# Kernel tuning notes

Measured on AMD Instinct MI355X. Metric: run time of the kernel, lower is better.

The kernel has to match this reference:

```python
import jax, jax.numpy as jnp
import numpy as np

N_EXPERTS = 9
MODEL_DIM = 256
NUM_HEADS = 4
N_TOKENS = 4096
LN_EPS = 1e-5


def setup_inputs() -> dict:
    key0 = jax.random.key(0)
    ks = jax.random.split(key0, 8)
    D, E = MODEL_DIM, N_EXPERTS
    x = jax.random.normal(ks[0], (N_TOKENS, D), dtype=jnp.float32)
    label = jax.random.randint(ks[1], (N_TOKENS,), 0, E, dtype=jnp.int64)
    s = 0.02
    Wq = jax.random.normal(ks[2], (E, D, D), dtype=jnp.float32) * s
    Wk = jax.random.normal(ks[3], (E, D, D), dtype=jnp.float32) * s
    Wv = jax.random.normal(ks[4], (E, D, D), dtype=jnp.float32) * s
    bq = jnp.zeros((E, D), dtype=jnp.float32)
    bk = jnp.zeros((E, D), dtype=jnp.float32)
    bv = jnp.zeros((E, D), dtype=jnp.float32)
    Wf = jax.random.normal(ks[5], (D, D), dtype=jnp.float32) * s
    bf = jnp.zeros((D,), dtype=jnp.float32)
    gamma = jnp.ones((D,), dtype=jnp.float32)
    beta = jnp.zeros((D,), dtype=jnp.float32)
    return {"x": x, "label": label, "Wq": Wq, "bq": bq, "Wk": Wk, "bk": bk,
            "Wv": Wv, "bv": bv, "Wf": Wf, "bf": bf, "gamma": gamma, "beta": beta}


def reference(x, label, Wq, bq, Wk, bk, Wv, bv, Wf, bf, gamma, beta):
    # v2 path: per-label expert QKV projection + within-label self-attention.
    N, D = x.shape
    H = NUM_HEADS
    dph = D // H  # dim_per_head = 64
    # NOTE: source uses scale = (dim_per_head // num_heads) ** -0.5
    scale = float((dph // H)) ** -0.5
    idx = jnp.arange(N)
    lbl = label.astype(jnp.int32)

    # Compute all 9 expert projections, then select per-token (dense dispatch).
    q = jnp.einsum('nd,edh->enh', x, Wq)[lbl, idx] + bq[lbl]  # [N, D]
    k = jnp.einsum('nd,edh->enh', x, Wk)[lbl, idx] + bk[lbl]
    v = jnp.einsum('nd,edh->enh', x, Wv)[lbl, idx] + bv[lbl]

    qh = q.reshape(N, H, dph)
    kh = k.reshape(N, H, dph)
    vh = v.reshape(N, H, dph)

    # Attention restricted to tokens with the same label (equivalent to the
    # per-label gather -> bmm -> scatter in the torch loop).
    scores = jnp.einsum('nhd,mhd->hnm', qh, kh) * scale  # [H, N, N]
    same = (lbl[:, None] == lbl[None, :])  # [N, N]
    scores = jnp.where(same[None, :, :], scores, -jnp.inf)
    attn = jax.nn.softmax(scores, axis=-1)
    ctx = jnp.einsum('hnm,mhd->nhd', attn, vh).reshape(N, D)

    out = ctx @ Wf + bf
    h = x + out  # residual is the (gathered) original key
    mean = jnp.mean(h, axis=-1, keepdims=True)
    var = jnp.mean(jnp.square(h - mean), axis=-1, keepdims=True)
    return gamma * (h - mean) / jnp.sqrt(var + LN_EPS) + beta
```

## Files before the change

kernel.cpp:

```cpp
#include <hip/hip_runtime.h>
#include <math.h>

#define N_TOK 4096
#define DIM 256
#define NHEAD 4
#define DPH 64
#define NEXP 9
#define SCALE 0.25f
#define TQ 16
#define MAXST 80
#define GPAD 4736
#define VPITCH 4736

typedef short s8 __attribute__((ext_vector_type(8)));
typedef short s4 __attribute__((ext_vector_type(4)));
typedef float f4 __attribute__((ext_vector_type(4)));

static __device__ __forceinline__ short f2bf(float f) {
  union { float f; unsigned u; } v;
  v.f = f;
  unsigned r = (v.u + 0x7FFFu + ((v.u >> 16) & 1u)) >> 16;
  return (short)r;
}

static __device__ __forceinline__ float wave_sum(float v) {
#pragma unroll
  for (int o = 32; o > 0; o >>= 1) v += __shfl_xor(v, o, 64);
  return v;
}

__global__ void k_build(const int* __restrict__ label, int* __restrict__ perm,
                        int* __restrict__ iperm, int* __restrict__ gs,
                        int* __restrict__ gep, int* __restrict__ st_e,
                        int* __restrict__ st_row, int* __restrict__ nstp) {
  __shared__ int cnt[NEXP];
  __shared__ int base[NEXP];
  int tid = threadIdx.x;
  if (tid < NEXP) cnt[tid] = 0;
  __syncthreads();
  for (int t = tid; t < N_TOK; t += 256) atomicAdd(&cnt[label[t]], 1);
  __syncthreads();
  if (tid == 0) {
    int run = 0, ns = 0;
    for (int e = 0; e < NEXP; e++) {
      gs[e] = run;
      base[e] = run;
      int end = run + cnt[e];
      gep[e] = end;
      for (int r = run; r < end; r += 64) { st_e[ns] = e; st_row[ns] = r; ns++; }
      run = (end + 63) & ~63;
    }
    *nstp = ns;
  }
  __syncthreads();
  for (int t = tid; t < N_TOK; t += 256) {
    int e = label[t];
    int pos = atomicAdd(&base[e], 1);
    perm[pos] = t;
    iperm[t] = pos;
  }
}

__global__ __launch_bounds__(256) void k_castx(const float* __restrict__ x,
                                               const int* __restrict__ perm,
                                               const int* __restrict__ gs,
                                               const int* __restrict__ gep,
                                               short* __restrict__ xb) {
  int grow = blockIdx.x * 64 + (threadIdx.x >> 2);
  int qd = (threadIdx.x & 3) * 64;
  bool valid = false;
#pragma unroll
  for (int e = 0; e < NEXP; e++) valid |= (grow >= gs[e] && grow < gep[e]);
  short* dst = xb + (size_t)grow * DIM + qd;
  if (valid) {
    const float* src = x + (size_t)perm[grow] * DIM + qd;
#pragma unroll
    for (int i = 0; i < 16; i++) {
      float4 v = *(const float4*)(src + i * 4);
      s4 o;
      o[0] = f2bf(v.x); o[1] = f2bf(v.y); o[2] = f2bf(v.z); o[3] = f2bf(v.w);
      *(s4*)(dst + i * 4) = o;
    }
  } else {
#pragma unroll
    for (int i = 0; i < 16; i++) *(s4*)(dst + i * 4) = (s4){0, 0, 0, 0};
  }
}

__global__ __launch_bounds__(256) void k_castw(const float* __restrict__ Wq,
                                               const float* __restrict__ Wk,
                                               const float* __restrict__ Wv,
                                               const float* __restrict__ Wf,
                                               short* __restrict__ WbT) {
  __shared__ short tile[64 * 68];
  int slab = blockIdx.y;
  const float* src;
  if (slab < 9) src = Wq + (size_t)slab * 65536;
  else if (slab < 18) src = Wk + (size_t)(slab - 9) * 65536;
  else if (slab < 27) src = Wv + (size_t)(slab - 18) * 65536;
  else src = Wf;
  int d0 = (blockIdx.x >> 2) * 64, h0 = (blockIdx.x & 3) * 64;
  int tid = threadIdx.x;
  int rl = tid >> 4;
  int hh = (tid & 15) * 4;
#pragma unroll
  for (int p = 0; p < 4; p++) {
    int dl = p * 16 + rl;
    float4 v = *(const float4*)(src + (size_t)(d0 + dl) * 256 + h0 + hh);
    s4 o;
    o[0] = f2bf(v.x); o[1] = f2bf(v.y); o[2] = f2bf(v.z); o[3] = f2bf(v.w);
    *(s4*)&tile[dl * 68 + hh] = o;
  }
  __syncthreads();
  int h = tid >> 2, dq = (tid & 3) * 16;
  s8 pa, pb;
#pragma unroll
  for (int i = 0; i < 8; i++) {
    pa[i] = tile[(dq + i) * 68 + h];
    pb[i] = tile[(dq + 8 + i) * 68 + h];
  }
  short* dst = WbT + (size_t)slab * 65536 + (size_t)(h0 + h) * 256 + d0 + dq;
  *(s8*)dst = pa;
  *(s8*)(dst + 8) = pb;
}

__global__ __launch_bounds__(256) void k_proj(
    const short* __restrict__ xb, const short* __restrict__ WbT,
    const float* __restrict__ bq, const float* __restrict__ bk,
    const float* __restrict__ bv, const int* __restrict__ st_e,
    const int* __restrict__ st_row, const int* __restrict__ nstp,
    short* __restrict__ qg, short* __restrict__ kg, short* __restrict__ vgT) {
  int b = blockIdx.x;
  if (b >= *nstp) return;
  int gy = blockIdx.y;
  int mtx = blockIdx.z;
  int e = st_e[b];
  int row0 = st_row[b];
  int tid = threadIdx.x, wl = tid >> 6, lane = tid & 63;
  int m = lane & 15, quad = lane >> 4;

  const short* Ap = xb + (size_t)(row0 + wl * 16 + m) * DIM + quad * 8;
  const short* Bp = WbT + (size_t)(mtx * 9 + e) * 65536 +
                    (size_t)(gy * 64 + m) * 256 + quad * 8;
  const float* bias = (mtx == 0) ? bq : (mtx == 1) ? bk : bv;

  s8 ac = *(const s8*)Ap;
  s8 bc[4];
#pragma unroll
  for (int t = 0; t < 4; t++) bc[t] = *(const s8*)(Bp + t * 16 * 256);

  f4 acc[4];
#pragma unroll
  for (int t = 0; t < 4; t++) acc[t] = (f4){0.f, 0.f, 0.f, 0.f};

#pragma unroll
  for (int kc = 0; kc < 8; kc++) {
    s8 an = ac;
    s8 bn[4] = {bc[0], bc[1], bc[2], bc[3]};
    if (kc < 7) {
      an = *(const s8*)(Ap + (kc + 1) * 32);
#pragma unroll
      for (int t = 0; t < 4; t++)
        bn[t] = *(const s8*)(Bp + t * 16 * 256 + (kc + 1) * 32);
    }
#pragma unroll
    for (int t = 0; t < 4; t++)
      acc[t] = __builtin_amdgcn_mfma_f32_16x16x32_bf16(ac, bc[t], acc[t], 0, 0, 0);
    ac = an;
#pragma unroll
    for (int t = 0; t < 4; t++) bc[t] = bn[t];
  }

#pragma unroll
  for (int t = 0; t < 4; t++) {
    int col = gy * 64 + t * 16 + m;
    float bs = bias[e * DIM + col];
#pragma unroll
    for (int r = 0; r < 4; r++) {
      int grow = row0 + wl * 16 + quad * 4 + r;
      short o = f2bf(acc[t][r] + bs);
      if (mtx == 2) vgT[(size_t)col * VPITCH + grow] = o;
      else if (mtx == 1) kg[(size_t)grow * DIM + col] = o;
      else qg[(size_t)grow * DIM + col] = o;
    }
  }
}

__global__ __launch_bounds__(256) void k_attn(
    const short* __restrict__ qg, const short* __restrict__ kg,
    const short* __restrict__ vgT, const int* __restrict__ gs,
    const int* __restrict__ gep, const int* __restrict__ st_e,
    const int* __restrict__ st_row, const int* __restrict__ nstp,
    short* __restrict__ cg) {
  int b = blockIdx.x;
  if (b >= *nstp) return;
  int h = blockIdx.y;
  int e = st_e[b];
  int row0 = st_row[b];
  int g0 = gs[e], kend = gep[e];

  int tid = threadIdx.x;
  int wl = tid >> 6;
  int lane = tid & 63;
  int m = lane & 15;
  int quad = lane >> 4;
  int r0 = tid >> 3;
  int c0 = (tid & 7) * 8;

  __shared__ short k_s[64 * 72];
  __shared__ short v_s[64 * 72];
  __shared__ short p_s[4 * 16 * 72];

  int qrow = row0 + wl * 16 + m;
  if (qrow >= kend) qrow = row0;
  s8 qf0 = *(const s8*)&qg[(size_t)qrow * DIM + h * DPH + quad * 8];
  s8 qf1 = *(const s8*)&qg[(size_t)qrow * DIM + h * DPH + 32 + quad * 8];

  f4 o_acc[4];
  float l_r[4];
#pragma unroll
  for (int t = 0; t < 4; t++) o_acc[t] = (f4){0.f, 0.f, 0.f, 0.f};
#pragma unroll
  for (int r = 0; r < 4; r++) l_r[r] = 0.f;

  s8 pk0, pk1, pv0, pv1;
#define PREF(JT)                                                            \
  do {                                                                      \
    pk0 = *(const s8*)&kg[(size_t)((JT) + r0) * DIM + h * DPH + c0];        \
    pk1 = *(const s8*)&kg[(size_t)((JT) + r0 + 32) * DIM + h * DPH + c0];   \
    pv0 = *(const s8*)&vgT[(size_t)(h * DPH + r0) * VPITCH + (JT) + c0];    \
    pv1 = *(const s8*)&vgT[(size_t)(h * DPH + r0 + 32) * VPITCH + (JT) + c0]; \
  } while (0)

  PREF(g0);
  for (int jt = g0; jt < kend; jt += 64) {
    __syncthreads();
    *(s8*)&k_s[r0 * 72 + c0] = pk0;
    *(s8*)&k_s[(r0 + 32) * 72 + c0] = pk1;
    *(s8*)&v_s[r0 * 72 + c0] = pv0;
    *(s8*)&v_s[(r0 + 32) * 72 + c0] = pv1;
    int jn = jt + 64;
    if (jn < kend) PREF(jn);
    __syncthreads();

    f4 s_acc[4];
#pragma unroll
    for (int t = 0; t < 4; t++) s_acc[t] = (f4){0.f, 0.f, 0.f, 0.f};
#pragma unroll
    for (int t = 0; t < 4; t++) {
      s8 kb0 = *(s8*)&k_s[(t * 16 + m) * 72 + quad * 8];
      s8 kb1 = *(s8*)&k_s[(t * 16 + m) * 72 + 32 + quad * 8];
      s_acc[t] = __builtin_amdgcn_mfma_f32_16x16x32_bf16(qf0, kb0, s_acc[t], 0, 0, 0);
      s_acc[t] = __builtin_amdgcn_mfma_f32_16x16x32_bf16(qf1, kb1, s_acc[t], 0, 0, 0);
    }

#pragma unroll
    for (int t = 0; t < 4; t++) {
      bool ok = (jt + t * 16 + m) < kend;
#pragma unroll
      for (int r = 0; r < 4; r++) {
        float p = ok ? __expf(s_acc[t][r] * SCALE) : 0.f;
        l_r[r] += p;
        p_s[(wl * 16 + quad * 4 + r) * 72 + t * 16 + m] = f2bf(p);
      }
    }

#pragma unroll
    for (int kk = 0; kk < 2; kk++) {
      s8 pa = *(s8*)&p_s[(wl * 16 + m) * 72 + kk * 32 + quad * 8];
#pragma unroll
      for (int t = 0; t < 4; t++) {
        s8 vb = *(s8*)&v_s[(t * 16 + m) * 72 + kk * 32 + quad * 8];
        o_acc[t] = __builtin_amdgcn_mfma_f32_16x16x32_bf16(pa, vb, o_acc[t], 0, 0, 0);
      }
    }
  }
#undef PREF

#pragma unroll
  for (int r = 0; r < 4; r++) {
    float lt = l_r[r];
#pragma unroll
    for (int o = 8; o > 0; o >>= 1) lt += __shfl_xor(lt, o, 64);
    float inv = 1.f / lt;
    int grow = row0 + wl * 16 + quad * 4 + r;
#pragma unroll
    for (int t = 0; t < 4; t++)
      cg[(size_t)grow * DIM + h * DPH + t * 16 + m] = f2bf(o_acc[t][r] * inv);
  }
}

__global__ __launch_bounds__(256) void k_out(
    const short* __restrict__ cg, const short* __restrict__ WbT,
    const float* __restrict__ x, const float* __restrict__ bfv,
    const float* __restrict__ gamma, const float* __restrict__ beta,
    const int* __restrict__ iperm, float* __restrict__ out) {
  int t0 = blockIdx.x * TQ;
  int tid = threadIdx.x, wl = tid >> 6, lane = tid & 63;
  int m = lane & 15, quad = lane >> 4;
  __shared__ float h_s[TQ * 260];

  const short* Ap = cg + (size_t)iperm[t0 + m] * DIM + quad * 8;
  const short* Bp = WbT + (size_t)27 * 65536 + (size_t)(wl * 64 + m) * 256 + quad * 8;

  s8 ac = *(const s8*)Ap;
  s8 bc[4];
#pragma unroll
  for (int t = 0; t < 4; t++) bc[t] = *(const s8*)(Bp + t * 16 * 256);

  f4 acc[4];
#pragma unroll
  for (int t = 0; t < 4; t++) acc[t] = (f4){0.f, 0.f, 0.f, 0.f};

#pragma unroll
  for (int kc = 0; kc < 8; kc++) {
    s8 an = ac;
    s8 bn[4] = {bc[0], bc[1], bc[2], bc[3]};
    if (kc < 7) {
      an = *(const s8*)(Ap + (kc + 1) * 32);
#pragma unroll
      for (int t = 0; t < 4; t++)
        bn[t] = *(const s8*)(Bp + t * 16 * 256 + (kc + 1) * 32);
    }
#pragma unroll
    for (int t = 0; t < 4; t++)
      acc[t] = __builtin_amdgcn_mfma_f32_16x16x32_bf16(ac, bc[t], acc[t], 0, 0, 0);
    ac = an;
#pragma unroll
    for (int t = 0; t < 4; t++) bc[t] = bn[t];
  }

#pragma unroll
  for (int t = 0; t < 4; t++) {
    int col = wl * 64 + t * 16 + m;
    float bs = bfv[col];
#pragma unroll
    for (int r = 0; r < 4; r++) h_s[(quad * 4 + r) * 260 + col] = acc[t][r] + bs;
  }
  __syncthreads();

  int w = tid >> 6;
#pragma unroll
  for (int rr = 0; rr < 4; rr++) {
    int row = w * 4 + rr;
    float hv[4];
#pragma unroll
    for (int k2 = 0; k2 < 4; k2++)
      hv[k2] = h_s[row * 260 + lane + 64 * k2] +
               x[(size_t)(t0 + row) * DIM + lane + 64 * k2];
    float sum = hv[0] + hv[1] + hv[2] + hv[3];
    float mean = wave_sum(sum) * (1.f / 256.f);
    float sq = 0.f;
#pragma unroll
    for (int k2 = 0; k2 < 4; k2++) {
      float dd = hv[k2] - mean;
      sq += dd * dd;
    }
    float var = wave_sum(sq) * (1.f / 256.f);
    float rstd = rsqrtf(var + 1e-5f);
#pragma unroll
    for (int k2 = 0; k2 < 4; k2++) {
      int c = lane + 64 * k2;
      out[(size_t)(t0 + row) * DIM + c] =
          gamma[c] * ((hv[k2] - mean) * rstd) + beta[c];
    }
  }
}

extern "C" void kernel_launch(void* const* d_in, const int* in_sizes, int n_in,
                              void* d_out, int out_size, void* d_ws,
                              size_t ws_size, hipStream_t stream) {
  const float* x = (const float*)d_in[0];
  const int* label = (const int*)d_in[1];
  const float* Wq = (const float*)d_in[2];
  const float* bq = (const float*)d_in[3];
  const float* Wk = (const float*)d_in[4];
  const float* bk = (const float*)d_in[5];
  const float* Wv = (const float*)d_in[6];
  const float* bv = (const float*)d_in[7];
  const float* Wf = (const float*)d_in[8];
  const float* bfv = (const float*)d_in[9];
  const float* gamma = (const float*)d_in[10];
  const float* beta = (const float*)d_in[11];
  float* out = (float*)d_out;

  int* perm = (int*)d_ws;
  int* iperm = perm + 8192;
  int* gs = iperm + 4096;
  int* gep = gs + 16;
  int* st_e = gep + 16;
  int* st_row = st_e + 128;
  int* nstp = st_row + 128;
  short* qg = (short*)((char*)d_ws + 65536);
  short* kg = qg + (size_t)GPAD * DIM;
  short* vgT = kg + (size_t)GPAD * DIM;
  short* WbT = vgT + (size_t)DIM * VPITCH;
  short* xb = WbT + (size_t)28 * 65536;
  short* cg = xb;

  hipLaunchKernelGGL(k_build, dim3(1), dim3(256), 0, stream, label, perm,
                     iperm, gs, gep, st_e, st_row, nstp);
  hipLaunchKernelGGL(k_castw, dim3(16, 28), dim3(256), 0, stream, Wq, Wk, Wv,
                     Wf, WbT);
  hipLaunchKernelGGL(k_castx, dim3(GPAD / 64), dim3(256), 0, stream, x, perm,
                     gs, gep, xb);
  hipLaunchKernelGGL(k_proj, dim3(MAXST, 4, 3), dim3(256), 0, stream, xb, WbT,
                     bq, bk, bv, st_e, st_row, nstp, qg, kg, vgT);
  hipLaunchKernelGGL(k_attn, dim3(MAXST, NHEAD), dim3(256), 0, stream, qg, kg,
                     vgT, gs, gep, st_e, st_row, nstp, cg);
  hipLaunchKernelGGL(k_out, dim3(N_TOK / TQ), dim3(256), 0, stream, cg, WbT, x,
                     bfv, gamma, beta, iperm, out);
}
```

Measured before the change: 147.6 us.

## Fuse all stages into one persistent kernel with software grid barriers

Replaces six separate kernel launches with a single persistent kernel of 256 blocks. Work items are handed out grid-stride and the stages are separated by atomic-counter grid barriers. The goal is to remove launch overhead and inter-kernel gaps. The cost is spin-wait barriers, reduced parallelism in the attention stage (nst*4 work items over 256 blocks), and block 0 doing label bucketing serially while the others cast weights. It relies on all 256 blocks being co-resident, and cg now gets its own buffer instead of aliasing xb.

```diff
diff --git a/kernel.cpp b/kernel.cpp
--- a/kernel.cpp
+++ b/kernel.cpp
@@ -7,10 +7,9 @@
 #define DPH 64
 #define NEXP 9
 #define SCALE 0.25f
-#define TQ 16
-#define MAXST 80
 #define GPAD 4736
 #define VPITCH 4736
+#define NB 256
 
 typedef short s8 __attribute__((ext_vector_type(8)));
 typedef short s4 __attribute__((ext_vector_type(4)));
@@ -29,340 +28,333 @@
   return v;
 }
 
-__global__ void k_build(const int* __restrict__ label, int* __restrict__ perm,
-                        int* __restrict__ iperm, int* __restrict__ gs,
-                        int* __restrict__ gep, int* __restrict__ st_e,
-                        int* __restrict__ st_row, int* __restrict__ nstp) {
-  __shared__ int cnt[NEXP];
-  __shared__ int base[NEXP];
+static __device__ __forceinline__ void gridbar(int* c, int target) {
+  __syncthreads();
+  if (threadIdx.x == 0) {
+    __threadfence();
+    __hip_atomic_fetch_add(c, 1, __ATOMIC_RELEASE, __HIP_MEMORY_SCOPE_AGENT);
+    while (__hip_atomic_load(c, __ATOMIC_ACQUIRE, __HIP_MEMORY_SCOPE_AGENT) <
+           target)
+      __builtin_amdgcn_s_sleep(2);
+    __threadfence();
+  }
+  __syncthreads();
+}
+
+__global__ __launch_bounds__(256) void k_fused(
+    const float* __restrict__ x, const int* __restrict__ label,
+    const float* __restrict__ Wq, const float* __restrict__ bq,
+    const float* __restrict__ Wk, const float* __restrict__ bk,
+    const float* __restrict__ Wv, const float* __restrict__ bv,
+    const float* __restrict__ Wf, const float* __restrict__ bfv,
+    const float* __restrict__ gamma, const float* __restrict__ beta,
+    int* __restrict__ cnt, int* __restrict__ perm, int* __restrict__ iperm,
+    int* __restrict__ gs, int* __restrict__ gep, int* __restrict__ st_e,
+    int* __restrict__ st_row, int* __restrict__ nstp, short* __restrict__ qg,
+    short* __restrict__ kg, short* __restrict__ vgT, short* __restrict__ WbT,
+    short* __restrict__ xb, short* __restrict__ cg, float* __restrict__ out) {
+  __shared__ __align__(16) char smem[27648];
+  __shared__ int cntL[NEXP], baseL[NEXP];
+
+  int b = blockIdx.x;
   int tid = threadIdx.x;
-  if (tid < NEXP) cnt[tid] = 0;
-  __syncthreads();
-  for (int t = tid; t < N_TOK; t += 256) atomicAdd(&cnt[label[t]], 1);
-  __syncthreads();
-  if (tid == 0) {
-    int run = 0, ns = 0;
-    for (int e = 0; e < NEXP; e++) {
-      gs[e] = run;
-      base[e] = run;
-      int end = run + cnt[e];
-      gep[e] = end;
-      for (int r = run; r < end; r += 64) { st_e[ns] = e; st_row[ns] = r; ns++; }
-      run = (end + 63) & ~63;
-    }
-    *nstp = ns;
-  }
-  __syncthreads();
-  for (int t = tid; t < N_TOK; t += 256) {
-    int e = label[t];
-    int pos = atomicAdd(&base[e], 1);
-    perm[pos] = t;
-    iperm[t] = pos;
-  }
-}
-
-__global__ __launch_bounds__(256) void k_castx(const float* __restrict__ x,
-                                               const int* __restrict__ perm,
-                                               const int* __restrict__ gs,
-                                               const int* __restrict__ gep,
-                                               short* __restrict__ xb) {
-  int grow = blockIdx.x * 64 + (threadIdx.x >> 2);
-  int qd = (threadIdx.x & 3) * 64;
-  bool valid = false;
-#pragma unroll
-  for (int e = 0; e < NEXP; e++) valid |= (grow >= gs[e] && grow < gep[e]);
-  short* dst = xb + (size_t)grow * DIM + qd;
-  if (valid) {
-    const float* src = x + (size_t)perm[grow] * DIM + qd;
-#pragma unroll
-    for (int i = 0; i < 16; i++) {
-      float4 v = *(const float4*)(src + i * 4);
-      s4 o;
-      o[0] = f2bf(v.x); o[1] = f2bf(v.y); o[2] = f2bf(v.z); o[3] = f2bf(v.w);
-      *(s4*)(dst + i * 4) = o;
+  int wl = tid >> 6, lane = tid & 63;
+  int m = lane & 15, quad = lane >> 4;
+
+  if (b == 0) {
+    if (tid < NEXP) cntL[tid] = 0;
+    __syncthreads();
+    for (int t = tid; t < N_TOK; t += 256) atomicAdd(&cntL[label[t]], 1);
+    __syncthreads();
+    if (tid == 0) {
+      int run = 0, ns = 0;
+      for (int e = 0; e < NEXP; e++) {
+        gs[e] = run;
+        baseL[e] = run;
+        int end = run + cntL[e];
+        gep[e] = end;
+        for (int r = run; r < end; r += 64) {
+          st_e[ns] = e;
+          st_row[ns] = r;
+          ns++;
+        }
+        run = (end + 63) & ~63;
+      }
+      *nstp = ns;
+    }
+    __syncthreads();
+    for (int t = tid; t < N_TOK; t += 256) {
+      int e = label[t];
+      int pos = atomicAdd(&baseL[e], 1);
+      perm[pos] = t;
+      iperm[t] = pos;
     }
   } else {
-#pragma unroll
-    for (int i = 0; i < 16; i++) *(s4*)(dst + i * 4) = (s4){0, 0, 0, 0};
-  }
-}
-
-__global__ __launch_bounds__(256) void k_castw(const float* __restrict__ Wq,
-                                               const float* __restrict__ Wk,
-                                               const float* __restrict__ Wv,
-                                               const float* __restrict__ Wf,
-                                               short* __restrict__ WbT) {
-  __shared__ short tile[64 * 68];
-  int slab = blockIdx.y;
-  const float* src;
-  if (slab < 9) src = Wq + (size_t)slab * 65536;
-  else if (slab < 18) src = Wk + (size_t)(slab - 9) * 65536;
-  else if (slab < 27) src = Wv + (size_t)(slab - 18) * 65536;
-  else src = Wf;
-  int d0 = (blockIdx.x >> 2) * 64, h0 = (blockIdx.x & 3) * 64;
-  int tid = threadIdx.x;
-  int rl = tid >> 4;
-  int hh = (tid & 15) * 4;
-#pragma unroll
-  for (int p = 0; p < 4; p++) {
-    int dl = p * 16 + rl;
-    float4 v = *(const float4*)(src + (size_t)(d0 + dl) * 256 + h0 + hh);
-    s4 o;
-    o[0] = f2bf(v.x); o[1] = f2bf(v.y); o[2] = f2bf(v.z); o[3] = f2bf(v.w);
-    *(s4*)&tile[dl * 68 + hh] = o;
-  }
-  __syncthreads();
-  int h = tid >> 2, dq = (tid & 3) * 16;
-  s8 pa, pb;
-#pragma unroll
-  for (int i = 0; i < 8; i++) {
-    pa[i] = tile[(dq + i) * 68 + h];
-    pb[i] = tile[(dq + 8 + i) * 68 + h];
-  }
-  short* dst = WbT + (size_t)slab * 65536 + (size_t)(h0 + h) * 256 + d0 + dq;
-  *(s8*)dst = pa;
-  *(s8*)(dst + 8) = pb;
-}
-
-__global__ __launch_bounds__(256) void k_proj(
-    const short* __restrict__ xb, const short* __restrict__ WbT,
-    const float* __restrict__ bq, const float* __restrict__ bk,
-    const float* __restrict__ bv, const int* __restrict__ st_e,
-    const int* __restrict__ st_row, const int* __restrict__ nstp,
-    short* __restrict__ qg, short* __restrict__ kg, short* __restrict__ vgT) {
-  int b = blockIdx.x;
-  if (b >= *nstp) return;
-  int gy = blockIdx.y;
-  int mtx = blockIdx.z;
-  int e = st_e[b];
-  int row0 = st_row[b];
-  int tid = threadIdx.x, wl = tid >> 6, lane = tid & 63;
-  int m = lane & 15, quad = lane >> 4;
-
-  const short* Ap = xb + (size_t)(row0 + wl * 16 + m) * DIM + quad * 8;
-  const short* Bp = WbT + (size_t)(mtx * 9 + e) * 65536 +
-                    (size_t)(gy * 64 + m) * 256 + quad * 8;
-  const float* bias = (mtx == 0) ? bq : (mtx == 1) ? bk : bv;
-
-  s8 ac = *(const s8*)Ap;
-  s8 bc[4];
-#pragma unroll
-  for (int t = 0; t < 4; t++) bc[t] = *(const s8*)(Bp + t * 16 * 256);
-
-  f4 acc[4];
-#pragma unroll
-  for (int t = 0; t < 4; t++) acc[t] = (f4){0.f, 0.f, 0.f, 0.f};
-
-#pragma unroll
-  for (int kc = 0; kc < 8; kc++) {
-    s8 an = ac;
-    s8 bn[4] = {bc[0], bc[1], bc[2], bc[3]};
-    if (kc < 7) {
-      an = *(const s8*)(Ap + (kc + 1) * 32);
+    short* tile = (short*)smem;
+    for (int vt = b - 1; vt < 448; vt += NB - 1) {
+      int slab = vt >> 4;
+      const float* src = (slab < 9)    ? Wq + (size_t)slab * 65536
+                         : (slab < 18) ? Wk + (size_t)(slab - 9) * 65536
+                         : (slab < 27) ? Wv + (size_t)(slab - 18) * 65536
+                                       : Wf;
+      int xy = vt & 15;
+      int d0 = (xy >> 2) * 64, h0 = (xy & 3) * 64;
+      int rl = tid >> 4;
+      int hh = (tid & 15) * 4;
+#pragma unroll
+      for (int p = 0; p < 4; p++) {
+        int dl = p * 16 + rl;
+        float4 v = *(const float4*)(src + (size_t)(d0 + dl) * 256 + h0 + hh);
+        s4 o;
+        o[0] = f2bf(v.x); o[1] = f2bf(v.y); o[2] = f2bf(v.z); o[3] = f2bf(v.w);
+        *(s4*)&tile[dl * 68 + hh] = o;
+      }
+      __syncthreads();
+      int h = tid >> 2, dq = (tid & 3) * 16;
+      s8 pa, pb;
+#pragma unroll
+      for (int i = 0; i < 8; i++) {
+        pa[i] = tile[(dq + i) * 68 + h];
+        pb[i] = tile[(dq + 8 + i) * 68 + h];
+      }
+      short* dst = WbT + (size_t)slab * 65536 + (size_t)(h0 + h) * 256 + d0 + dq;
+      *(s8*)dst = pa;
+      *(s8*)(dst + 8) = pb;
+      __syncthreads();
+    }
+  }
+  gridbar(cnt, NB);
+
+  for (int vb = b; vb < GPAD / 64; vb += NB) {
+    int grow = vb * 64 + (tid >> 2);
+    int qd = (tid & 3) * 64;
+    bool valid = false;
+#pragma unroll
+    for (int e = 0; e < NEXP; e++) valid |= (grow >= gs[e] && grow < gep[e]);
+    short* dst = xb + (size_t)grow * DIM + qd;
+    if (valid) {
+      const float* src = x + (size_t)perm[grow] * DIM + qd;
+#pragma unroll
+      for (int i = 0; i < 16; i++) {
+        float4 v = *(const float4*)(src + i * 4);
+        s4 o;
+        o[0] = f2bf(v.x); o[1] = f2bf(v.y); o[2] = f2bf(v.z); o[3] = f2bf(v.w);
+        *(s4*)(dst + i * 4) = o;
+      }
+    } else {
+#pragma unroll
+      for (int i = 0; i < 16; i++) *(s4*)(dst + i * 4) = (s4){0, 0, 0, 0};
+    }
+  }
+  gridbar(cnt, 2 * NB);
+  int nst = *nstp;
+
+  for (int vb = b; vb < nst * 12; vb += NB) {
+    int st = vb / 12, rem = vb - st * 12;
+    int gy = rem & 3, mtx = rem >> 2;
+    int e = st_e[st], row0 = st_row[st];
+    const short* Ap = xb + (size_t)(row0 + wl * 16 + m) * DIM + quad * 8;
+    const short* Bp = WbT + (size_t)(mtx * 9 + e) * 65536 +
+                      (size_t)(gy * 64 + m) * 256 + quad * 8;
+    const float* bias = (mtx == 0) ? bq : (mtx == 1) ? bk : bv;
+
+    s8 ac = *(const s8*)Ap;
+    s8 bc[4];
+#pragma unroll
+    for (int t = 0; t < 4; t++) bc[t] = *(const s8*)(Bp + t * 16 * 256);
+    f4 acc[4];
+#pragma unroll
+    for (int t = 0; t < 4; t++) acc[t] = (f4){0.f, 0.f, 0.f, 0.f};
+#pragma unroll
+    for (int kc = 0; kc < 8; kc++) {
+      s8 an = ac;
+      s8 bn[4] = {bc[0], bc[1], bc[2], bc[3]};
+      if (kc < 7) {
+        an = *(const s8*)(Ap + (kc + 1) * 32);
+#pragma unroll
+        for (int t = 0; t < 4; t++)
+          bn[t] = *(const s8*)(Bp + t * 16 * 256 + (kc + 1) * 32);
+      }
 #pragma unroll
       for (int t = 0; t < 4; t++)
-        bn[t] = *(const s8*)(Bp + t * 16 * 256 + (kc + 1) * 32);
-    }
-#pragma unroll
-    for (int t = 0; t < 4; t++)
-      acc[t] = __builtin_amdgcn_mfma_f32_16x16x32_bf16(ac, bc[t], acc[t], 0, 0, 0);
-    ac = an;
-#pragma unroll
-    for (int t = 0; t < 4; t++) bc[t] = bn[t];
-  }
-
-#pragma unroll
-  for (int t = 0; t < 4; t++) {
-    int col = gy * 64 + t * 16 + m;
-    float bs = bias[e * DIM + col];
-#pragma unroll
-    for (int r = 0; r < 4; r++) {
-      int grow = row0 + wl * 16 + quad * 4 + r;
-      short o = f2bf(acc[t][r] + bs);
-      if (mtx == 2) vgT[(size_t)col * VPITCH + grow] = o;
-      else if (mtx == 1) kg[(size_t)grow * DIM + col] = o;
-      else qg[(size_t)grow * DIM + col] = o;
-    }
-  }
-}
-
-__global__ __launch_bounds__(256) void k_attn(
-    const short* __restrict__ qg, const short* __restrict__ kg,
-    const short* __restrict__ vgT, const int* __restrict__ gs,
-    const int* __restrict__ gep, const int* __restrict__ st_e,
-    const int* __restrict__ st_row, const int* __restrict__ nstp,
-    short* __restrict__ cg) {
-  int b = blockIdx.x;
-  if (b >= *nstp) return;
-  int h = blockIdx.y;
-  int e = st_e[b];
-  int row0 = st_row[b];
-  int g0 = gs[e], kend = gep[e];
-
-  int tid = threadIdx.x;
-  int wl = tid >> 6;
-  int lane = tid & 63;
-  int m = lane & 15;
-  int quad = lane >> 4;
-  int r0 = tid >> 3;
-  int c0 = (tid & 7) * 8;
-
-  __shared__ short k_s[64 * 72];
-  __shared__ short v_s[64 * 72];
-  __shared__ short p_s[4 * 16 * 72];
-
-  int qrow = row0 + wl * 16 + m;
-  if (qrow >= kend) qrow = row0;
-  s8 qf0 = *(const s8*)&qg[(size_t)qrow * DIM + h * DPH + quad * 8];
-  s8 qf1 = *(const s8*)&qg[(size_t)qrow * DIM + h * DPH + 32 + quad * 8];
-
-  f4 o_acc[4];
-  float l_r[4];
-#pragma unroll
-  for (int t = 0; t < 4; t++) o_acc[t] = (f4){0.f, 0.f, 0.f, 0.f};
-#pragma unroll
-  for (int r = 0; r < 4; r++) l_r[r] = 0.f;
-
-  s8 pk0, pk1, pv0, pv1;
-#define PREF(JT)                                                            \
-  do {                                                                      \
-    pk0 = *(const s8*)&kg[(size_t)((JT) + r0) * DIM + h * DPH + c0];        \
-    pk1 = *(const s8*)&kg[(size_t)((JT) + r0 + 32) * DIM + h * DPH + c0];   \
-    pv0 = *(const s8*)&vgT[(size_t)(h * DPH + r0) * VPITCH + (JT) + c0];    \
+        acc[t] = __builtin_amdgcn_mfma_f32_16x16x32_bf16(ac, bc[t], acc[t], 0, 0, 0);
+      ac = an;
+#pragma unroll
+      for (int t = 0; t < 4; t++) bc[t] = bn[t];
+    }
+#pragma unroll
+    for (int t = 0; t < 4; t++) {
+      int col = gy * 64 + t * 16 + m;
+      float bs = bias[e * DIM + col];
+#pragma unroll
+      for (int r = 0; r < 4; r++) {
+        int grow = row0 + wl * 16 + quad * 4 + r;
+        short o = f2bf(acc[t][r] + bs);
+        if (mtx == 2) vgT[(size_t)col * VPITCH + grow] = o;
+        else if (mtx == 1) kg[(size_t)grow * DIM + col] = o;
+        else qg[(size_t)grow * DIM + col] = o;
+      }
+    }
+  }
+  gridbar(cnt, 3 * NB);
+
+  {
+    short* k_s = (short*)smem;
+    short* v_s = (short*)(smem + 9216);
+    short* p_s = (short*)(smem + 18432);
+    int r0 = tid >> 3;
+    int c0 = (tid & 7) * 8;
+    for (int vb = b; vb < nst * 4; vb += NB) {
+      int st = vb >> 2, h = vb & 3;
+      int e = st_e[st], row0 = st_row[st];
+      int g0 = gs[e], kend = gep[e];
+
+      int qrow = row0 + wl * 16 + m;
+      if (qrow >= kend) qrow = row0;
+      s8 qf0 = *(const s8*)&qg[(size_t)qrow * DIM + h * DPH + quad * 8];
+      s8 qf1 = *(const s8*)&qg[(size_t)qrow * DIM + h * DPH + 32 + quad * 8];
+
+      f4 o_acc[4];
+      float l_r[4];
+#pragma unroll
+      for (int t = 0; t < 4; t++) o_acc[t] = (f4){0.f, 0.f, 0.f, 0.f};
+#pragma unroll
+      for (int r = 0; r < 4; r++) l_r[r] = 0.f;
+
+      s8 pk0, pk1, pv0, pv1;
+#define PREF(JT)                                                              \
+  do {                                                                        \
+    pk0 = *(const s8*)&kg[(size_t)((JT) + r0) * DIM + h * DPH + c0];          \
+    pk1 = *(const s8*)&kg[(size_t)((JT) + r0 + 32) * DIM + h * DPH + c0];     \
+    pv0 = *(const s8*)&vgT[(size_t)(h * DPH + r0) * VPITCH + (JT) + c0];      \
     pv1 = *(const s8*)&vgT[(size_t)(h * DPH + r0 + 32) * VPITCH + (JT) + c0]; \
   } while (0)
 
-  PREF(g0);
-  for (int jt = g0; jt < kend; jt += 64) {
+      PREF(g0);
+      for (int jt = g0; jt < kend; jt += 64) {
+        __syncthreads();
+        *(s8*)&k_s[r0 * 72 + c0] = pk0;
+        *(s8*)&k_s[(r0 + 32) * 72 + c0] = pk1;
+        *(s8*)&v_s[r0 * 72 + c0] = pv0;
+        *(s8*)&v_s[(r0 + 32) * 72 + c0] = pv1;
+        int jn = jt + 64;
+        if (jn < kend) PREF(jn);
+        __syncthreads();
+
+        f4 s_acc[4];
+#pragma unroll
+        for (int t = 0; t < 4; t++) s_acc[t] = (f4){0.f, 0.f, 0.f, 0.f};
+#pragma unroll
+        for (int t = 0; t < 4; t++) {
+          s8 kb0 = *(s8*)&k_s[(t * 16 + m) * 72 + quad * 8];
+          s8 kb1 = *(s8*)&k_s[(t * 16 + m) * 72 + 32 + quad * 8];
+          s_acc[t] = __builtin_amdgcn_mfma_f32_16x16x32_bf16(qf0, kb0, s_acc[t], 0, 0, 0);
+          s_acc[t] = __builtin_amdgcn_mfma_f32_16x16x32_bf16(qf1, kb1, s_acc[t], 0, 0, 0);
+        }
+
+#pragma unroll
+        for (int t = 0; t < 4; t++) {
+          bool ok = (jt + t * 16 + m) < kend;
+#pragma unroll
+          for (int r = 0; r < 4; r++) {
+            float p = ok ? __expf(s_acc[t][r] * SCALE) : 0.f;
+            l_r[r] += p;
+            p_s[(wl * 16 + quad * 4 + r) * 72 + t * 16 + m] = f2bf(p);
+          }
+        }
+
+#pragma unroll
+        for (int kk = 0; kk < 2; kk++) {
+          s8 pa = *(s8*)&p_s[(wl * 16 + m) * 72 + kk * 32 + quad * 8];
+#pragma unroll
+          for (int t = 0; t < 4; t++) {
+            s8 vb2 = *(s8*)&v_s[(t * 16 + m) * 72 + kk * 32 + quad * 8];
+            o_acc[t] = __builtin_amdgcn_mfma_f32_16x16x32_bf16(pa, vb2, o_acc[t], 0, 0, 0);
+          }
+        }
+      }
+#undef PREF
+
+#pragma unroll
+      for (int r = 0; r < 4; r++) {
+        float lt = l_r[r];
+#pragma unroll
+        for (int o = 8; o > 0; o >>= 1) lt += __shfl_xor(lt, o, 64);
+        float inv = 1.f / lt;
+        int grow = row0 + wl * 16 + quad * 4 + r;
+#pragma unroll
+        for (int t = 0; t < 4; t++)
+          cg[(size_t)grow * DIM + h * DPH + t * 16 + m] = f2bf(o_acc[t][r] * inv);
+      }
+    }
+  }
+  gridbar(cnt, 4 * NB);
+
+  {
+    float* h_s = (float*)smem;
+    int t0 = b * 16;
+    const short* Ap = cg + (size_t)iperm[t0 + m] * DIM + quad * 8;
+    const short* Bp = WbT + (size_t)27 * 65536 + (size_t)(wl * 64 + m) * 256 + quad * 8;
+
+    s8 ac = *(const s8*)Ap;
+    s8 bc[4];
+#pragma unroll
+    for (int t = 0; t < 4; t++) bc[t] = *(const s8*)(Bp + t * 16 * 256);
+    f4 acc[4];
+#pragma unroll
+    for (int t = 0; t < 4; t++) acc[t] = (f4){0.f, 0.f, 0.f, 0.f};
+#pragma unroll
+    for (int kc = 0; kc < 8; kc++) {
+      s8 an = ac;
+      s8 bn[4] = {bc[0], bc[1], bc[2], bc[3]};
+      if (kc < 7) {
+        an = *(const s8*)(Ap + (kc + 1) * 32);
+#pragma unroll
+        for (int t = 0; t < 4; t++)
+          bn[t] = *(const s8*)(Bp + t * 16 * 256 + (kc + 1) * 32);
+      }
+#pragma unroll
+      for (int t = 0; t < 4; t++)
+        acc[t] = __builtin_amdgcn_mfma_f32_16x16x32_bf16(ac, bc[t], acc[t], 0, 0, 0);
+      ac = an;
+#pragma unroll
+      for (int t = 0; t < 4; t++) bc[t] = bn[t];
+    }
+
+#pragma unroll
+    for (int t = 0; t < 4; t++) {
+      int col = wl * 64 + t * 16 + m;
+      float bs = bfv[col];
+#pragma unroll
+      for (int r = 0; r < 4; r++)
+        h_s[(quad * 4 + r) * 260 + col] = acc[t][r] + bs;
+    }
     __syncthreads();
-    *(s8*)&k_s[r0 * 72 + c0] = pk0;
-    *(s8*)&k_s[(r0 + 32) * 72 + c0] = pk1;
-    *(s8*)&v_s[r0 * 72 + c0] = pv0;
-    *(s8*)&v_s[(r0 + 32) * 72 + c0] = pv1;
-    int jn = jt + 64;
-    if (jn < kend) PREF(jn);
-    __syncthreads();
-
-    f4 s_acc[4];
-#pragma unroll
-    for (int t = 0; t < 4; t++) s_acc[t] = (f4){0.f, 0.f, 0.f, 0.f};
-#pragma unroll
-    for (int t = 0; t < 4; t++) {
-      s8 kb0 = *(s8*)&k_s[(t * 16 + m) * 72 + quad * 8];
-      s8 kb1 = *(s8*)&k_s[(t * 16 + m) * 72 + 32 + quad * 8];
-      s_acc[t] = __builtin_amdgcn_mfma_f32_16x16x32_bf16(qf0, kb0, s_acc[t], 0, 0, 0);
-      s_acc[t] = __builtin_amdgcn_mfma_f32_16x16x32_bf16(qf1, kb1, s_acc[t], 0, 0, 0);
-    }
-
-#pragma unroll
-    for (int t = 0; t < 4; t++) {
-      bool ok = (jt + t * 16 + m) < kend;
-#pragma unroll
-      for (int r = 0; r < 4; r++) {
-        float p = ok ? __expf(s_acc[t][r] * SCALE) : 0.f;
-        l_r[r] += p;
-        p_s[(wl * 16 + quad * 4 + r) * 72 + t * 16 + m] = f2bf(p);
-      }
-    }
-
-#pragma unroll
-    for (int kk = 0; kk < 2; kk++) {
-      s8 pa = *(s8*)&p_s[(wl * 16 + m) * 72 + kk * 32 + quad * 8];
-#pragma unroll
-      for (int t = 0; t < 4; t++) {
-        s8 vb = *(s8*)&v_s[(t * 16 + m) * 72 + kk * 32 + quad * 8];
-        o_acc[t] = __builtin_amdgcn_mfma_f32_16x16x32_bf16(pa, vb, o_acc[t], 0, 0, 0);
-      }
-    }
-  }
-#undef PREF
-
-#pragma unroll
-  for (int r = 0; r < 4; r++) {
-    float lt = l_r[r];
-#pragma unroll
-    for (int o = 8; o > 0; o >>= 1) lt += __shfl_xor(lt, o, 64);
-    float inv = 1.f / lt;
-    int grow = row0 + wl * 16 + quad * 4 + r;
-#pragma unroll
-    for (int t = 0; t < 4; t++)
-      cg[(size_t)grow * DIM + h * DPH + t * 16 + m] = f2bf(o_acc[t][r] * inv);
-  }
-}
-
-__global__ __launch_bounds__(256) void k_out(
-    const short* __restrict__ cg, const short* __restrict__ WbT,
-    const float* __restrict__ x, const float* __restrict__ bfv,
-    const float* __restrict__ gamma, const float* __restrict__ beta,
-    const int* __restrict__ iperm, float* __restrict__ out) {
-  int t0 = blockIdx.x * TQ;
-  int tid = threadIdx.x, wl = tid >> 6, lane = tid & 63;
-  int m = lane & 15, quad = lane >> 4;
-  __shared__ float h_s[TQ * 260];
-
-  const short* Ap = cg + (size_t)iperm[t0 + m] * DIM + quad * 8;
-  const short* Bp = WbT + (size_t)27 * 65536 + (size_t)(wl * 64 + m) * 256 + quad * 8;
-
-  s8 ac = *(const s8*)Ap;
-  s8 bc[4];
-#pragma unroll
-  for (int t = 0; t < 4; t++) bc[t] = *(const s8*)(Bp + t * 16 * 256);
-
-  f4 acc[4];
-#pragma unroll
-  for (int t = 0; t < 4; t++) acc[t] = (f4){0.f, 0.f, 0.f, 0.f};
-
-#pragma unroll
-  for (int kc = 0; kc < 8; kc++) {
-    s8 an = ac;
-    s8 bn[4] = {bc[0], bc[1], bc[2], bc[3]};
-    if (kc < 7) {
-      an = *(const s8*)(Ap + (kc + 1) * 32);
-#pragma unroll
-      for (int t = 0; t < 4; t++)
-        bn[t] = *(const s8*)(Bp + t * 16 * 256 + (kc + 1) * 32);
-    }
-#pragma unroll
-    for (int t = 0; t < 4; t++)
-      acc[t] = __builtin_amdgcn_mfma_f32_16x16x32_bf16(ac, bc[t], acc[t], 0, 0, 0);
-    ac = an;
-#pragma unroll
-    for (int t = 0; t < 4; t++) bc[t] = bn[t];
-  }
-
-#pragma unroll
-  for (int t = 0; t < 4; t++) {
-    int col = wl * 64 + t * 16 + m;
-    float bs = bfv[col];
-#pragma unroll
-    for (int r = 0; r < 4; r++) h_s[(quad * 4 + r) * 260 + col] = acc[t][r] + bs;
-  }
-  __syncthreads();
-
-  int w = tid >> 6;
-#pragma unroll
-  for (int rr = 0; rr < 4; rr++) {
-    int row = w * 4 + rr;
-    float hv[4];
-#pragma unroll
-    for (int k2 = 0; k2 < 4; k2++)
-      hv[k2] = h_s[row * 260 + lane + 64 * k2] +
-               x[(size_t)(t0 + row) * DIM + lane + 64 * k2];
-    float sum = hv[0] + hv[1] + hv[2] + hv[3];
-    float mean = wave_sum(sum) * (1.f / 256.f);
-    float sq = 0.f;
-#pragma unroll
-    for (int k2 = 0; k2 < 4; k2++) {
-      float dd = hv[k2] - mean;
-      sq += dd * dd;
-    }
-    float var = wave_sum(sq) * (1.f / 256.f);
-    float rstd = rsqrtf(var + 1e-5f);
-#pragma unroll
-    for (int k2 = 0; k2 < 4; k2++) {
-      int c = lane + 64 * k2;
-      out[(size_t)(t0 + row) * DIM + c] =
-          gamma[c] * ((hv[k2] - mean) * rstd) + beta[c];
+
+#pragma unroll
+    for (int rr = 0; rr < 4; rr++) {
+      int row = wl * 4 + rr;
+      float hv[4];
+#pragma unroll
+      for (int k2 = 0; k2 < 4; k2++)
+        hv[k2] = h_s[row * 260 + lane + 64 * k2] +
+                 x[(size_t)(t0 + row) * DIM + lane + 64 * k2];
+      float sum = hv[0] + hv[1] + hv[2] + hv[3];
+      float mean = wave_sum(sum) * (1.f / 256.f);
+      float sq = 0.f;
+#pragma unroll
+      for (int k2 = 0; k2 < 4; k2++) {
+        float dd = hv[k2] - mean;
+        sq += dd * dd;
+      }
+      float var = wave_sum(sq) * (1.f / 256.f);
+      float rstd = rsqrtf(var + 1e-5f);
+#pragma unroll
+      for (int k2 = 0; k2 < 4; k2++) {
+        int c = lane + 64 * k2;
+        out[(size_t)(t0 + row) * DIM + c] =
+            gamma[c] * ((hv[k2] - mean) * rstd) + beta[c];
+      }
     }
   }
 }
@@ -384,8 +376,9 @@
   const float* beta = (const float*)d_in[11];
   float* out = (float*)d_out;
 
-  int* perm = (int*)d_ws;
-  int* iperm = perm + 8192;
+  int* cnt = (int*)d_ws;
+  int* perm = cnt + 64;
+  int* iperm = perm + 4800;
   int* gs = iperm + 4096;
   int* gep = gs + 16;
   int* st_e = gep + 16;
@@ -396,18 +389,11 @@
   short* vgT = kg + (size_t)GPAD * DIM;
   short* WbT = vgT + (size_t)DIM * VPITCH;
   short* xb = WbT + (size_t)28 * 65536;
-  short* cg = xb;
-
-  hipLaunchKernelGGL(k_build, dim3(1), dim3(256), 0, stream, label, perm,
-                     iperm, gs, gep, st_e, st_row, nstp);
-  hipLaunchKernelGGL(k_castw, dim3(16, 28), dim3(256), 0, stream, Wq, Wk, Wv,
-                     Wf, WbT);
-  hipLaunchKernelGGL(k_castx, dim3(GPAD / 64), dim3(256), 0, stream, x, perm,
-                     gs, gep, xb);
-  hipLaunchKernelGGL(k_proj, dim3(MAXST, 4, 3), dim3(256), 0, stream, xb, WbT,
-                     bq, bk, bv, st_e, st_row, nstp, qg, kg, vgT);
-  hipLaunchKernelGGL(k_attn, dim3(MAXST, NHEAD), dim3(256), 0, stream, qg, kg,
-                     vgT, gs, gep, st_e, st_row, nstp, cg);
-  hipLaunchKernelGGL(k_out, dim3(N_TOK / TQ), dim3(256), 0, stream, cg, WbT, x,
-                     bfv, gamma, beta, iperm, out);
-}
+  short* cg = xb + (size_t)GPAD * DIM;
+
+  hipMemsetAsync(cnt, 0, 256, stream);
+  hipLaunchKernelGGL(k_fused, dim3(NB), dim3(256), 0, stream, x, label, Wq, bq,
+                     Wk, bk, Wv, bv, Wf, bfv, gamma, beta, cnt, perm, iperm,
+                     gs, gep, st_e, st_row, nstp, qg, kg, vgT, WbT, xb, cg,
+                     out);
+}
```

Measured after the change: 329.4 us. 123% more time.
